# Optimization experiments

Hardware: AMD Instinct MI355X
Metric: run time of the kernel (lower is better)

The kernel has to match this reference:

```python
import jax, jax.numpy as jnp
import numpy as np

N, E, D, L, G, C = 20000, 320000, 512, 6, 64, 10
EPS = 1e-5


def setup_inputs() -> dict:
    key = jax.random.key(0)
    ks = jax.random.split(key, 8)
    s = 0.05  # small init scale to keep activations sane across 6 layers
    x = jax.random.normal(ks[0], (N, D), jnp.float32)
    edge_index = jax.random.randint(ks[1], (2, E), 0, N, jnp.int32)
    batch = jnp.sort(jax.random.randint(ks[2], (N,), 0, G, jnp.int32))
    W_rel = jax.random.normal(ks[3], (L, D, D), jnp.float32) * s
    b_rel = jnp.zeros((L, D), jnp.float32)
    W_root = jax.random.normal(ks[4], (L, D, D), jnp.float32) * s
    gamma = jnp.ones((L, D), jnp.float32)
    beta = jnp.zeros((L, D), jnp.float32)
    lin_w = jax.random.normal(ks[5], (D, C), jnp.float32) * s
    lin_b = jnp.zeros((C,), jnp.float32)
    return {"x": x, "edge_index": edge_index, "batch": batch,
            "W_rel": W_rel, "b_rel": b_rel, "W_root": W_root,
            "gamma": gamma, "beta": beta, "lin_w": lin_w, "lin_b": lin_b}


def reference(x, edge_index, batch, W_rel, b_rel, W_root, gamma, beta, lin_w, lin_b):
    # PyG GraphConv (aggr='add'): out = segment_sum(x[src] -> dst) @ W_rel + b_rel + x @ W_root
    src, dst = edge_index[0], edge_index[1]
    n = x.shape[0]
    for l in range(W_rel.shape[0]):  # 6 structurally identical layers
        agg = jax.ops.segment_sum(x[src], dst, num_segments=n)  # [N, D]
        h = agg @ W_rel[l] + b_rel[l] + x @ W_root[l]
        # BatchNorm1d in training mode: biased batch statistics over nodes
        mu = jnp.mean(h, axis=0)
        var = jnp.mean(jnp.square(h - mu), axis=0)
        x = jax.nn.relu((h - mu) * jax.lax.rsqrt(var + EPS) * gamma[l] + beta[l])
    # global_mean_pool over per-node graph ids
    sums = jax.ops.segment_sum(x, batch, num_segments=G)              # [G, D]
    counts = jax.ops.segment_sum(jnp.ones((n,), x.dtype), batch, num_segments=G)
    pooled = sums / jnp.maximum(counts, 1.0)[:, None]
    return pooled @ lin_w + lin_b  # [G, C]
```

## Files before the change

kernel.cpp:

```cpp
#include <hip/hip_runtime.h>


typedef unsigned short u16;
typedef unsigned int u32;
typedef __attribute__((ext_vector_type(8))) short bf16x8;
typedef __attribute__((ext_vector_type(4))) float f32x4;

#define DFEAT 512
#define KDIM 1024
#define NLAYER 6
#define NGRAPH 64
#define NCLS 10
#define BN_EPS 1e-5f

__device__ __forceinline__ float bf_lo(u32 u) { union { u32 i; float f; } v; v.i = u << 16; return v.f; }
__device__ __forceinline__ float bf_hi(u32 u) { union { u32 i; float f; } v; v.i = u & 0xFFFF0000u; return v.f; }
__device__ __forceinline__ u16 f2bf(float f) {
  union { float f; u32 i; } v; v.f = f;
  u32 r = v.i + 0x7FFFu + ((v.i >> 16) & 1u);
  return (u16)(r >> 16);
}
__device__ __forceinline__ u32 pack2(float lo, float hi) {
  return (u32)f2bf(lo) | ((u32)f2bf(hi) << 16);
}

__device__ __forceinline__ void gload_lds16(const u16* g, u16* lds_base) {
  __builtin_amdgcn_global_load_lds(
      (const __attribute__((address_space(1))) u32*)g,
      (__attribute__((address_space(3))) u32*)lds_base, 16, 0, 0);
}

__global__ void hist_kernel(const int* __restrict__ ei, int* __restrict__ counts, int E) {
  int e = blockIdx.x * 256 + threadIdx.x;
  if (e < E) atomicAdd(&counts[ei[E + e]], 1);
}

__global__ __launch_bounds__(1024) void scan_kernel(const int* __restrict__ counts,
                                                    int* __restrict__ row_ptr, int n) {
  __shared__ int buf[1024];
  int tid = threadIdx.x;
  int carry = 0;
  for (int base = 0; base < n; base += 1024) {
    int i = base + tid;
    int v = (i < n) ? counts[i] : 0;
    buf[tid] = v;
    __syncthreads();
    int x = v;
    for (int off = 1; off < 1024; off <<= 1) {
      int t = (tid >= off) ? buf[tid - off] : 0;
      __syncthreads();
      x += t;
      buf[tid] = x;
      __syncthreads();
    }
    if (i < n) row_ptr[i] = carry + x - v;
    int tot = buf[1023];
    __syncthreads();
    carry += tot;
  }
  if (tid == 0) row_ptr[n] = carry;
}

__global__ void scatter_kernel(const int* __restrict__ ei, int* __restrict__ cursor,
                               int* __restrict__ csr_src, int E) {
  int e = blockIdx.x * 256 + threadIdx.x;
  if (e < E) {
    int d = ei[E + e];
    int pos = atomicAdd(&cursor[d], 1);
    csr_src[pos] = ei[e];
  }
}

__global__ void wconv_kernel(const float* __restrict__ Wrel, const float* __restrict__ Wroot,
                             u16* __restrict__ Wt) {
  int idx = blockIdx.x * 256 + threadIdx.x;
  int k = idx & 1023;
  int n = (idx >> 10) & 511;
  int l = idx >> 19;
  float v = (k < DFEAT) ? Wrel[((size_t)l * DFEAT + k) * DFEAT + n]
                        : Wroot[((size_t)l * DFEAT + (k - DFEAT)) * DFEAT + n];
  Wt[idx] = f2bf(v);
}

__global__ void xconv_kernel(const float* __restrict__ x, u16* __restrict__ A, int M) {
  int idx = blockIdx.x * 256 + threadIdx.x;
  int row = idx >> 7;
  int c4 = (idx & 127) * 4;
  if (row >= M) return;
  float4 v = *(const float4*)&x[(size_t)row * DFEAT + c4];
  uint2 o; o.x = pack2(v.x, v.y); o.y = pack2(v.z, v.w);
  *(uint2*)&A[(size_t)row * KDIM + DFEAT + c4] = o;
}

__device__ __forceinline__ void add8(uint4 v, float* a) {
  a[0] += bf_lo(v.x); a[1] += bf_hi(v.x);
  a[2] += bf_lo(v.y); a[3] += bf_hi(v.y);
  a[4] += bf_lo(v.z); a[5] += bf_hi(v.z);
  a[6] += bf_lo(v.w); a[7] += bf_hi(v.w);
}

__global__ __launch_bounds__(256) void gather_kernel(u16* __restrict__ A,
                                                     const int* __restrict__ row_ptr,
                                                     const int* __restrict__ csr_src, int n) {
  int b = blockIdx.x;
  int slice = b & 7;
  int grp = b >> 3;
  int wid = threadIdx.x >> 6, lane = threadIdx.x & 63;
  int dsub = lane >> 3, fl = lane & 7;
  int dst = grp * 32 + wid * 8 + dsub;
  if (dst >= n) return;
  int cc = slice * 64 + fl * 8;
  const u16* Sx = A + DFEAT;
  int beg = row_ptr[dst], end = row_ptr[dst + 1];
  float a[8] = {};
  int e = beg;
  for (; e + 7 < end; e += 8) {
    uint4 v0 = *(const uint4*)&Sx[(size_t)csr_src[e + 0] * KDIM + cc];
    uint4 v1 = *(const uint4*)&Sx[(size_t)csr_src[e + 1] * KDIM + cc];
    uint4 v2 = *(const uint4*)&Sx[(size_t)csr_src[e + 2] * KDIM + cc];
    uint4 v3 = *(const uint4*)&Sx[(size_t)csr_src[e + 3] * KDIM + cc];
    uint4 v4 = *(const uint4*)&Sx[(size_t)csr_src[e + 4] * KDIM + cc];
    uint4 v5 = *(const uint4*)&Sx[(size_t)csr_src[e + 5] * KDIM + cc];
    uint4 v6 = *(const uint4*)&Sx[(size_t)csr_src[e + 6] * KDIM + cc];
    uint4 v7 = *(const uint4*)&Sx[(size_t)csr_src[e + 7] * KDIM + cc];
    add8(v0, a); add8(v1, a); add8(v2, a); add8(v3, a);
    add8(v4, a); add8(v5, a); add8(v6, a); add8(v7, a);
  }
  for (; e + 3 < end; e += 4) {
    uint4 v0 = *(const uint4*)&Sx[(size_t)csr_src[e + 0] * KDIM + cc];
    uint4 v1 = *(const uint4*)&Sx[(size_t)csr_src[e + 1] * KDIM + cc];
    uint4 v2 = *(const uint4*)&Sx[(size_t)csr_src[e + 2] * KDIM + cc];
    uint4 v3 = *(const uint4*)&Sx[(size_t)csr_src[e + 3] * KDIM + cc];
    add8(v0, a); add8(v1, a); add8(v2, a); add8(v3, a);
  }
  for (; e < end; ++e) {
    uint4 v = *(const uint4*)&Sx[(size_t)csr_src[e] * KDIM + cc];
    add8(v, a);
  }
  uint4 o;
  o.x = pack2(a[0], a[1]); o.y = pack2(a[2], a[3]);
  o.z = pack2(a[4], a[5]); o.w = pack2(a[6], a[7]);
  *(uint4*)&A[(size_t)dst * KDIM + cc] = o;
}

#define BM 128
#define BN 128
#define BK 64
#define CSTR 132
__global__ __launch_bounds__(256, 4) void gemm_kernel(const u16* __restrict__ A,
                                                      const u16* __restrict__ Bt,
                                                      const float* __restrict__ bias,
                                                      u16* __restrict__ Hb,
                                                      float* __restrict__ sums, int M) {
  const int lin = blockIdx.x;
  const int bx = ((lin >> 5) << 3) + (lin & 7);
  const int by = (lin >> 3) & 3;
  const int m0 = bx * BM;
  if (m0 >= M) return;
  const int n0 = by * BN;

  __shared__ u16 smem[BM * CSTR];
  __shared__ float sred[2 * BN];
  u16* As = smem;
  u16* Bs = smem + BM * BK;
  const int tid = threadIdx.x;
  const int wid = tid >> 6, lane = tid & 63;
  const int wm = wid >> 1, wn = wid & 1;
  const int l16 = lane & 15, quad = lane >> 4;

  if (tid < 2 * BN) sred[tid] = 0.f;

  const int dr = lane >> 3;
  const int gcol = ((lane & 7) ^ dr) * 8;
  int arow[4], brow[4];
#pragma unroll
  for (int t = 0; t < 4; t++) {
    int r = wid * 32 + t * 8 + dr;
    int ar = m0 + r; if (ar >= M) ar = M - 1;
    arow[t] = ar;
    brow[t] = n0 + r;
  }

  f32x4 acc[4][4] = {};

  for (int k0 = 0; k0 < KDIM; k0 += BK) {
    __syncthreads();
#pragma unroll
    for (int t = 0; t < 4; t++)
      gload_lds16(&A[(size_t)arow[t] * KDIM + k0 + gcol], &As[(wid * 32 + t * 8) * BK]);
#pragma unroll
    for (int t = 0; t < 4; t++)
      gload_lds16(&Bt[(size_t)brow[t] * KDIM + k0 + gcol], &Bs[(wid * 32 + t * 8) * BK]);
    __syncthreads();
    bf16x8 af[2][4], bfr[2][4];
#pragma unroll
    for (int h = 0; h < 2; h++) {
      int slot = ((h * 4 + quad) ^ (l16 & 7)) * 8;
#pragma unroll
      for (int i = 0; i < 4; i++) {
        af[h][i]  = *(const bf16x8*)&As[(wm * 64 + i * 16 + l16) * BK + slot];
        bfr[h][i] = *(const bf16x8*)&Bs[(wn * 64 + i * 16 + l16) * BK + slot];
      }
    }
#pragma unroll
    for (int h = 0; h < 2; h++)
#pragma unroll
      for (int i = 0; i < 4; i++)
#pragma unroll
        for (int j = 0; j < 4; j++)
          acc[i][j] = __builtin_amdgcn_mfma_f32_16x16x32_bf16(af[h][i], bfr[h][j], acc[i][j], 0, 0, 0);
  }

  __syncthreads();

#pragma unroll
  for (int j = 0; j < 4; j++) {
    int colt = wn * 64 + j * 16 + l16;
    float bv = bias[n0 + colt];
    float s = 0.f, s2 = 0.f;
#pragma unroll
    for (int i = 0; i < 4; i++) {
      int rbase = wm * 64 + i * 16 + quad * 4;
#pragma unroll
      for (int r = 0; r < 4; r++) {
        int rowt = rbase + r;
        float v = acc[i][j][r] + bv;
        smem[rowt * CSTR + colt] = f2bf(v);
        if (m0 + rowt < M) { s += v; s2 += v * v; }
      }
    }
    s  += __shfl_xor(s, 16);  s  += __shfl_xor(s, 32);
    s2 += __shfl_xor(s2, 16); s2 += __shfl_xor(s2, 32);
    if (quad == 0) {
      atomicAdd(&sred[colt], s);
      atomicAdd(&sred[BN + colt], s2);
    }
  }
  __syncthreads();

  const int rsub = tid >> 4;
  const int c8 = (tid & 15) * 8;
#pragma unroll
  for (int it = 0; it < 8; it++) {
    int rowt = it * 16 + rsub;
    int grow = m0 + rowt;
    if (grow < M) {
      uint4 v = *(const uint4*)&smem[rowt * CSTR + c8];
      *(uint4*)&Hb[(size_t)grow * DFEAT + n0 + c8] = v;
    }
  }
  if (tid < BN) {
    atomicAdd(&sums[n0 + tid], sred[tid]);
    atomicAdd(&sums[DFEAT + n0 + tid], sred[BN + tid]);
  }
}

__global__ void norm_kernel(const u16* __restrict__ Hb, const float* __restrict__ sums,
                            const float* __restrict__ gamma, const float* __restrict__ beta,
                            u16* __restrict__ A, int M, float invN) {
  int idx = blockIdx.x * 256 + threadIdx.x;
  int row = idx >> 7;
  int c4 = (idx & 127) * 4;
  if (row >= M) return;
  float sc[4], sh[4];
#pragma unroll
  for (int j = 0; j < 4; j++) {
    int c = c4 + j;
    float mu = sums[c] * invN;
    float var = sums[DFEAT + c] * invN - mu * mu;
    float s = gamma[c] * rsqrtf(var + BN_EPS);
    sc[j] = s;
    sh[j] = beta[c] - mu * s;
  }
  uint2 h = *(const uint2*)&Hb[(size_t)row * DFEAT + c4];
  float x0 = fmaxf(bf_lo(h.x) * sc[0] + sh[0], 0.f);
  float x1 = fmaxf(bf_hi(h.x) * sc[1] + sh[1], 0.f);
  float x2 = fmaxf(bf_lo(h.y) * sc[2] + sh[2], 0.f);
  float x3 = fmaxf(bf_hi(h.y) * sc[3] + sh[3], 0.f);
  uint2 o; o.x = pack2(x0, x1); o.y = pack2(x2, x3);
  *(uint2*)&A[(size_t)row * KDIM + DFEAT + c4] = o;
}

__device__ __forceinline__ int lower_bound_dev(const int* a, int n, int v) {
  int lo = 0, hi = n;
  while (lo < hi) { int mid = (lo + hi) >> 1; if (a[mid] < v) lo = mid + 1; else hi = mid; }
  return lo;
}

__global__ __launch_bounds__(1024) void pool_kernel(const u16* __restrict__ Hb,
                                                    const float* __restrict__ sums,
                                                    const float* __restrict__ gamma,
                                                    const float* __restrict__ beta,
                                                    const int* __restrict__ batch,
                                                    float* __restrict__ pooled, int n, float invN) {
  __shared__ float red[DFEAT];
  int g = blockIdx.x;
  int tid = threadIdx.x;
  if (tid < DFEAT) red[tid] = 0.f;
  int lo = lower_bound_dev(batch, n, g);
  int hi = lower_bound_dev(batch, n, g + 1);
  int rowOff = tid >> 6, lane = tid & 63;
  int c0 = lane * 8;
  float sc[8], sh[8];
#pragma unroll
  for (int j = 0; j < 8; j++) {
    int c = c0 + j;
    float mu = sums[c] * invN;
    float var = sums[DFEAT + c] * invN - mu * mu;
    float s = gamma[c] * rsqrtf(var + BN_EPS);
    sc[j] = s;
    sh[j] = beta[c] - mu * s;
  }
  float a[8] = {};
  for (int r = lo + rowOff; r < hi; r += 16) {
    uint4 v = *(const uint4*)&Hb[(size_t)r * DFEAT + c0];
    float e0 = bf_lo(v.x), e1 = bf_hi(v.x), e2 = bf_lo(v.y), e3 = bf_hi(v.y);
    float e4 = bf_lo(v.z), e5 = bf_hi(v.z), e6 = bf_lo(v.w), e7 = bf_hi(v.w);
    a[0] += fmaxf(e0 * sc[0] + sh[0], 0.f); a[1] += fmaxf(e1 * sc[1] + sh[1], 0.f);
    a[2] += fmaxf(e2 * sc[2] + sh[2], 0.f); a[3] += fmaxf(e3 * sc[3] + sh[3], 0.f);
    a[4] += fmaxf(e4 * sc[4] + sh[4], 0.f); a[5] += fmaxf(e5 * sc[5] + sh[5], 0.f);
    a[6] += fmaxf(e6 * sc[6] + sh[6], 0.f); a[7] += fmaxf(e7 * sc[7] + sh[7], 0.f);
  }
  __syncthreads();
#pragma unroll
  for (int j = 0; j < 8; j++) atomicAdd(&red[c0 + j], a[j]);
  __syncthreads();
  if (tid < DFEAT) pooled[g * DFEAT + tid] = red[tid] / fmaxf((float)(hi - lo), 1.0f);
}

__global__ __launch_bounds__(64) void final_kernel(const float* __restrict__ pooled,
                                                   const float* __restrict__ lin_w,
                                                   const float* __restrict__ lin_b,
                                                   float* __restrict__ out) {
  int g = blockIdx.x;
  int lane = threadIdx.x;
  float acc[NCLS] = {};
  float4 p0 = *(const float4*)&pooled[g * DFEAT + lane * 8];
  float4 p1 = *(const float4*)&pooled[g * DFEAT + lane * 8 + 4];
  float pv[8] = {p0.x, p0.y, p0.z, p0.w, p1.x, p1.y, p1.z, p1.w};
#pragma unroll
  for (int j = 0; j < 8; j++) {
    int k = lane * 8 + j;
#pragma unroll
    for (int c = 0; c < NCLS; c++) acc[c] += pv[j] * lin_w[k * NCLS + c];
  }
#pragma unroll
  for (int off = 32; off > 0; off >>= 1)
#pragma unroll
    for (int c = 0; c < NCLS; c++) acc[c] += __shfl_down(acc[c], off);
  if (lane == 0)
#pragma unroll
    for (int c = 0; c < NCLS; c++) out[g * NCLS + c] = acc[c] + lin_b[c];
}

extern "C" void kernel_launch(void* const* d_in, const int* in_sizes, int n_in,
                              void* d_out, int out_size, void* d_ws, size_t ws_size,
                              hipStream_t stream) {
  const float* x      = (const float*)d_in[0];
  const int*   ei     = (const int*)d_in[1];
  const int*   batch  = (const int*)d_in[2];
  const float* W_rel  = (const float*)d_in[3];
  const float* b_rel  = (const float*)d_in[4];
  const float* W_root = (const float*)d_in[5];
  const float* gamma  = (const float*)d_in[6];
  const float* beta   = (const float*)d_in[7];
  const float* lin_w  = (const float*)d_in[8];
  const float* lin_b  = (const float*)d_in[9];
  float* out = (float*)d_out;

  const int N = in_sizes[0] / DFEAT;
  const int E = in_sizes[1] / 2;

  char* p = (char*)d_ws;
  u16*   A       = (u16*)p;    p += (size_t)N * KDIM * 2;
  u16*   Hb      = (u16*)p;    p += (size_t)N * DFEAT * 2;
  u16*   Wt      = (u16*)p;    p += (size_t)NLAYER * DFEAT * KDIM * 2;
  int*   row_ptr = (int*)p;    p += ((size_t)(N + 1) * 4 + 15) / 16 * 16;
  int*   cursor  = (int*)p;    p += (size_t)N * 4;
  int*   csr_src = (int*)p;    p += (size_t)E * 4;
  float* sums    = (float*)p;  p += (size_t)NLAYER * 2 * DFEAT * 4;
  float* pooled  = (float*)p;  p += (size_t)NGRAPH * DFEAT * 4;

  const float invN = 1.0f / (float)N;

  hipMemsetAsync(cursor, 0, (size_t)N * 4, stream);
  hipMemsetAsync(sums, 0, (size_t)NLAYER * 2 * DFEAT * 4, stream);

  hist_kernel<<<(E + 255) / 256, 256, 0, stream>>>(ei, cursor, E);
  scan_kernel<<<1, 1024, 0, stream>>>(cursor, row_ptr, N);
  hipMemcpyAsync(cursor, row_ptr, (size_t)N * 4, hipMemcpyDeviceToDevice, stream);
  scatter_kernel<<<(E + 255) / 256, 256, 0, stream>>>(ei, cursor, csr_src, E);

  wconv_kernel<<<(NLAYER * DFEAT * KDIM) / 256, 256, 0, stream>>>(W_rel, W_root, Wt);
  xconv_kernel<<<(N * 128 + 255) / 256, 256, 0, stream>>>(x, A, N);

  const int ngrp = (N + 31) / 32;
  const int gather_grid = ngrp * 8;
  const int gemm_rows = (N + BM - 1) / BM;
  const int gemm_grid = ((gemm_rows + 7) / 8) * 8 * 4;

  for (int l = 0; l < NLAYER; ++l) {
    float* sums_l = sums + (size_t)l * 2 * DFEAT;
    gather_kernel<<<gather_grid, 256, 0, stream>>>(A, row_ptr, csr_src, N);
    gemm_kernel<<<gemm_grid, 256, 0, stream>>>(A, Wt + (size_t)l * DFEAT * KDIM,
                                               b_rel + (size_t)l * DFEAT, Hb, sums_l, N);
    if (l < NLAYER - 1)
      norm_kernel<<<(N * 128 + 255) / 256, 256, 0, stream>>>(
          Hb, sums_l, gamma + (size_t)l * DFEAT, beta + (size_t)l * DFEAT, A, N, invN);
  }

  pool_kernel<<<NGRAPH, 1024, 0, stream>>>(Hb, sums + (size_t)(NLAYER - 1) * 2 * DFEAT,
                                           gamma + (size_t)(NLAYER - 1) * DFEAT,
                                           beta + (size_t)(NLAYER - 1) * DFEAT,
                                           batch, pooled, N, invN);
  final_kernel<<<NGRAPH, 64, 0, stream>>>(pooled, lin_w, lin_b, out);
}
```

Before: 631.9 us.

## Switch GEMM to 32x32x16 MFMA tiles and stage gather indices in LDS

The GEMM inner loop now uses 32x32x16 bf16 MFMA instructions with a 2x2 accumulator grid per wave instead of 4x4 tiles of 16x16x32. This cuts LDS fragment loads per MFMA and improves operand reuse, and the epilogue is remapped to the new accumulator layout. Separately, the gather kernel preloads each block's CSR source indices into shared memory, so the dependent index loads come from LDS rather than global memory. That adds a sync and LDS use, with a fallback path when a block's edge count exceeds the capacity.

```diff
diff --git a/kernel.cpp b/kernel.cpp
--- a/kernel.cpp
+++ b/kernel.cpp
@@ -4,7 +4,7 @@
 typedef unsigned short u16;
 typedef unsigned int u32;
 typedef __attribute__((ext_vector_type(8))) short bf16x8;
-typedef __attribute__((ext_vector_type(4))) float f32x4;
+typedef __attribute__((ext_vector_type(16))) float f32x16;
 
 #define DFEAT 512
 #define KDIM 1024
@@ -99,43 +99,57 @@
   a[6] += bf_lo(v.w); a[7] += bf_hi(v.w);
 }
 
+#define GCAP 6144
 __global__ __launch_bounds__(256) void gather_kernel(u16* __restrict__ A,
                                                      const int* __restrict__ row_ptr,
                                                      const int* __restrict__ csr_src, int n) {
+  __shared__ int sidx[GCAP];
   int b = blockIdx.x;
   int slice = b & 7;
   int grp = b >> 3;
-  int wid = threadIdx.x >> 6, lane = threadIdx.x & 63;
+  int tid = threadIdx.x;
+  int r0 = grp * 32;
+  int rend = (r0 + 32 < n) ? (r0 + 32) : n;
+  int wbeg = row_ptr[r0], wend = row_ptr[rend];
+  int cnt = wend - wbeg;
+  bool lds_ok = (cnt <= GCAP);
+  if (lds_ok)
+    for (int t = tid; t < cnt; t += 256) sidx[t] = csr_src[wbeg + t];
+  __syncthreads();
+
+  int wid = tid >> 6, lane = tid & 63;
   int dsub = lane >> 3, fl = lane & 7;
-  int dst = grp * 32 + wid * 8 + dsub;
+  int dst = r0 + wid * 8 + dsub;
   if (dst >= n) return;
   int cc = slice * 64 + fl * 8;
-  const u16* Sx = A + DFEAT;
-  int beg = row_ptr[dst], end = row_ptr[dst + 1];
+  const u16* Sx = A + DFEAT + cc;
+  int db = row_ptr[dst], de = row_ptr[dst + 1];
   float a[8] = {};
-  int e = beg;
-  for (; e + 7 < end; e += 8) {
-    uint4 v0 = *(const uint4*)&Sx[(size_t)csr_src[e + 0] * KDIM + cc];
-    uint4 v1 = *(const uint4*)&Sx[(size_t)csr_src[e + 1] * KDIM + cc];
-    uint4 v2 = *(const uint4*)&Sx[(size_t)csr_src[e + 2] * KDIM + cc];
-    uint4 v3 = *(const uint4*)&Sx[(size_t)csr_src[e + 3] * KDIM + cc];
-    uint4 v4 = *(const uint4*)&Sx[(size_t)csr_src[e + 4] * KDIM + cc];
-    uint4 v5 = *(const uint4*)&Sx[(size_t)csr_src[e + 5] * KDIM + cc];
-    uint4 v6 = *(const uint4*)&Sx[(size_t)csr_src[e + 6] * KDIM + cc];
-    uint4 v7 = *(const uint4*)&Sx[(size_t)csr_src[e + 7] * KDIM + cc];
-    add8(v0, a); add8(v1, a); add8(v2, a); add8(v3, a);
-    add8(v4, a); add8(v5, a); add8(v6, a); add8(v7, a);
-  }
-  for (; e + 3 < end; e += 4) {
-    uint4 v0 = *(const uint4*)&Sx[(size_t)csr_src[e + 0] * KDIM + cc];
-    uint4 v1 = *(const uint4*)&Sx[(size_t)csr_src[e + 1] * KDIM + cc];
-    uint4 v2 = *(const uint4*)&Sx[(size_t)csr_src[e + 2] * KDIM + cc];
-    uint4 v3 = *(const uint4*)&Sx[(size_t)csr_src[e + 3] * KDIM + cc];
-    add8(v0, a); add8(v1, a); add8(v2, a); add8(v3, a);
-  }
-  for (; e < end; ++e) {
-    uint4 v = *(const uint4*)&Sx[(size_t)csr_src[e] * KDIM + cc];
-    add8(v, a);
+  if (lds_ok) {
+    int e = db - wbeg, ee = de - wbeg;
+    for (; e + 7 < ee; e += 8) {
+      int s0 = sidx[e + 0], s1 = sidx[e + 1], s2 = sidx[e + 2], s3 = sidx[e + 3];
+      int s4 = sidx[e + 4], s5 = sidx[e + 5], s6 = sidx[e + 6], s7 = sidx[e + 7];
+      uint4 v0 = *(const uint4*)&Sx[(size_t)s0 * KDIM];
+      uint4 v1 = *(const uint4*)&Sx[(size_t)s1 * KDIM];
+      uint4 v2 = *(const uint4*)&Sx[(size_t)s2 * KDIM];
+      uint4 v3 = *(const uint4*)&Sx[(size_t)s3 * KDIM];
+      uint4 v4 = *(const uint4*)&Sx[(size_t)s4 * KDIM];
+      uint4 v5 = *(const uint4*)&Sx[(size_t)s5 * KDIM];
+      uint4 v6 = *(const uint4*)&Sx[(size_t)s6 * KDIM];
+      uint4 v7 = *(const uint4*)&Sx[(size_t)s7 * KDIM];
+      add8(v0, a); add8(v1, a); add8(v2, a); add8(v3, a);
+      add8(v4, a); add8(v5, a); add8(v6, a); add8(v7, a);
+    }
+    for (; e < ee; ++e) {
+      uint4 v = *(const uint4*)&Sx[(size_t)sidx[e] * KDIM];
+      add8(v, a);
+    }
+  } else {
+    for (int e = db; e < de; ++e) {
+      uint4 v = *(const uint4*)&Sx[(size_t)csr_src[e] * KDIM];
+      add8(v, a);
+    }
   }
   uint4 o;
   o.x = pack2(a[0], a[1]); o.y = pack2(a[2], a[3]);
@@ -166,7 +180,7 @@
   const int tid = threadIdx.x;
   const int wid = tid >> 6, lane = tid & 63;
   const int wm = wid >> 1, wn = wid & 1;
-  const int l16 = lane & 15, quad = lane >> 4;
+  const int l31 = lane & 31, half = lane >> 5;
 
   if (tid < 2 * BN) sred[tid] = 0.f;
 
@@ -181,7 +195,7 @@
     brow[t] = n0 + r;
   }
 
-  f32x4 acc[4][4] = {};
+  f32x16 acc[2][2] = {};
 
   for (int k0 = 0; k0 < KDIM; k0 += BK) {
     __syncthreads();
@@ -192,46 +206,41 @@
     for (int t = 0; t < 4; t++)
       gload_lds16(&Bt[(size_t)brow[t] * KDIM + k0 + gcol], &Bs[(wid * 32 + t * 8) * BK]);
     __syncthreads();
-    bf16x8 af[2][4], bfr[2][4];
-#pragma unroll
-    for (int h = 0; h < 2; h++) {
-      int slot = ((h * 4 + quad) ^ (l16 & 7)) * 8;
-#pragma unroll
-      for (int i = 0; i < 4; i++) {
-        af[h][i]  = *(const bf16x8*)&As[(wm * 64 + i * 16 + l16) * BK + slot];
-        bfr[h][i] = *(const bf16x8*)&Bs[(wn * 64 + i * 16 + l16) * BK + slot];
-      }
-    }
-#pragma unroll
-    for (int h = 0; h < 2; h++)
-#pragma unroll
-      for (int i = 0; i < 4; i++)
-#pragma unroll
-        for (int j = 0; j < 4; j++)
-          acc[i][j] = __builtin_amdgcn_mfma_f32_16x16x32_bf16(af[h][i], bfr[h][j], acc[i][j], 0, 0, 0);
+#pragma unroll
+    for (int ks = 0; ks < 4; ks++) {
+      int slot = ((ks * 2 + half) ^ (l31 & 7)) * 8;
+      bf16x8 a0 = *(const bf16x8*)&As[(wm * 64 + l31) * BK + slot];
+      bf16x8 a1 = *(const bf16x8*)&As[(wm * 64 + 32 + l31) * BK + slot];
+      bf16x8 b0 = *(const bf16x8*)&Bs[(wn * 64 + l31) * BK + slot];
+      bf16x8 b1 = *(const bf16x8*)&Bs[(wn * 64 + 32 + l31) * BK + slot];
+      acc[0][0] = __builtin_amdgcn_mfma_f32_32x32x16_bf16(a0, b0, acc[0][0], 0, 0, 0);
+      acc[0][1] = __builtin_amdgcn_mfma_f32_32x32x16_bf16(a0, b1, acc[0][1], 0, 0, 0);
+      acc[1][0] = __builtin_amdgcn_mfma_f32_32x32x16_bf16(a1, b0, acc[1][0], 0, 0, 0);
+      acc[1][1] = __builtin_amdgcn_mfma_f32_32x32x16_bf16(a1, b1, acc[1][1], 0, 0, 0);
+    }
   }
 
   __syncthreads();
 
 #pragma unroll
-  for (int j = 0; j < 4; j++) {
-    int colt = wn * 64 + j * 16 + l16;
+  for (int nt = 0; nt < 2; nt++) {
+    int colt = wn * 64 + nt * 32 + l31;
     float bv = bias[n0 + colt];
     float s = 0.f, s2 = 0.f;
 #pragma unroll
-    for (int i = 0; i < 4; i++) {
-      int rbase = wm * 64 + i * 16 + quad * 4;
-#pragma unroll
-      for (int r = 0; r < 4; r++) {
-        int rowt = rbase + r;
-        float v = acc[i][j][r] + bv;
+    for (int mt = 0; mt < 2; mt++) {
+      int rbase = wm * 64 + mt * 32 + half * 4;
+#pragma unroll
+      for (int reg = 0; reg < 16; reg++) {
+        int rowt = rbase + (reg & 3) + 8 * (reg >> 2);
+        float v = acc[mt][nt][reg] + bv;
         smem[rowt * CSTR + colt] = f2bf(v);
         if (m0 + rowt < M) { s += v; s2 += v * v; }
       }
     }
-    s  += __shfl_xor(s, 16);  s  += __shfl_xor(s, 32);
-    s2 += __shfl_xor(s2, 16); s2 += __shfl_xor(s2, 32);
-    if (quad == 0) {
+    s  += __shfl_xor(s, 32);
+    s2 += __shfl_xor(s2, 32);
+    if (half == 0) {
       atomicAdd(&sred[colt], s);
       atomicAdd(&sred[BN + colt], s2);
     }
```

New measurement: 615.1 us. 1.03x faster.
